# Kernel tuning notes

Hardware: AMD Instinct MI355X
Metric: run time of the kernel (lower is better)

Reference implementation:

```python
import jax, jax.numpy as jnp
import numpy as np

NUM_SECTIONS = 8192
EMBED_DIM = 768
NUM_HEADS = 12
D_K = 64
TOTAL_DIM = NUM_HEADS * D_K  # 768
M_MISSING = 2048
N_EXIST = 6144


def setup_inputs() -> dict:
    key = jax.random.key(0)
    ks = jax.random.split(key, 9)
    ehr = jax.random.normal(ks[0], (NUM_SECTIONS, EMBED_DIM), dtype=jnp.float32)
    # disjoint split of section indices (as in real missing/existing sections)
    perm = jax.random.permutation(ks[1], NUM_SECTIONS)
    missing_indices = perm[:M_MISSING].astype(jnp.int64) if jax.config.jax_enable_x64 else perm[:M_MISSING].astype(jnp.int32)
    exist_indices = perm[M_MISSING:M_MISSING + N_EXIST].astype(missing_indices.dtype)
    s = 1.0 / np.sqrt(EMBED_DIM)
    Wq = jax.random.normal(ks[2], (EMBED_DIM, TOTAL_DIM), dtype=jnp.float32) * s
    Wk = jax.random.normal(ks[3], (EMBED_DIM, TOTAL_DIM), dtype=jnp.float32) * s
    Wv = jax.random.normal(ks[4], (EMBED_DIM, TOTAL_DIM), dtype=jnp.float32) * s
    bq = jax.random.normal(ks[5], (TOTAL_DIM,), dtype=jnp.float32) * 0.01
    bk = jax.random.normal(ks[6], (TOTAL_DIM,), dtype=jnp.float32) * 0.01
    bv = jax.random.normal(ks[7], (TOTAL_DIM,), dtype=jnp.float32) * 0.01
    cooc_bias = jax.random.normal(ks[8], (NUM_HEADS, NUM_SECTIONS, D_K), dtype=jnp.float32)
    return {"ehr_embeddings": ehr, "exist_indices": exist_indices,
            "missing_indices": missing_indices, "Wq": Wq, "bq": bq,
            "Wk": Wk, "bk": bk, "Wv": Wv, "bv": bv, "cooc_bias": cooc_bias}


def reference(ehr_embeddings, exist_indices, missing_indices, Wq, bq, Wk, bk, Wv, bv, cooc_bias):
    M = missing_indices.shape[0]
    N = exist_indices.shape[0]
    missing_emb = ehr_embeddings[missing_indices]   # [M, E]
    exist_emb = ehr_embeddings[exist_indices]       # [N, E]
    # Q/K/V projections, split into heads: [H, M|N, d_k]
    q = (missing_emb @ Wq + bq).reshape(M, NUM_HEADS, D_K).transpose(1, 0, 2)
    k = (exist_emb @ Wk + bk).reshape(N, NUM_HEADS, D_K).transpose(1, 0, 2)
    v = (exist_emb @ Wv + bv).reshape(N, NUM_HEADS, D_K).transpose(1, 0, 2)
    scores = jnp.einsum('hmd,hnd->hmn', q, k) / jnp.sqrt(jnp.float32(D_K))
    # learned section co-occurrence bias
    missing_bias = cooc_bias[:, missing_indices, :]  # [H, M, d_k]
    exist_bias = cooc_bias[:, exist_indices, :]      # [H, N, d_k]
    scores = scores + jnp.einsum('hmd,hnd->hmn', missing_bias, exist_bias)
    attn = jax.nn.softmax(scores, axis=-1)
    out = jnp.einsum('hmn,hnd->hmd', attn, v)        # [H, M, d_k]
    out = out.transpose(1, 0, 2).reshape(M, TOTAL_DIM)
    return ehr_embeddings.at[missing_indices].set(out)
```

## Files before the change

### kernel.cpp

```cpp
#include <hip/hip_runtime.h>

typedef __attribute__((ext_vector_type(8))) short short8;
typedef __attribute__((ext_vector_type(8))) _Float16 half8;
typedef __attribute__((ext_vector_type(4))) float f32x4;
typedef __attribute__((ext_vector_type(16))) float f32x16;
typedef __attribute__((ext_vector_type(4))) unsigned short us4;
typedef __attribute__((ext_vector_type(4))) unsigned int u32x4;

#define MFMA16(a,b,c)  __builtin_amdgcn_mfma_f32_16x16x32_bf16(a,b,c,0,0,0)
#define MFMA32(a,b,c)  __builtin_amdgcn_mfma_f32_32x32x16_bf16(a,b,c,0,0,0)
#define MFMA32H(a,b,c) __builtin_amdgcn_mfma_f32_32x32x16_f16(a,b,c,0,0,0)

#define EMBED 768
#define HEADS 12
#define DK 64
#define M_MISS 2048
#define N_EX 6144
#define NSEC 8192
#define DPHY 128
#define QSC 0.125f
#define THR 7.0f

#define GLOAD16(g, l) __builtin_amdgcn_global_load_lds( \
    (const __attribute__((address_space(1))) unsigned int*)(g), \
    (__attribute__((address_space(3))) unsigned int*)(l), 16, 0, 0)

__device__ __forceinline__ unsigned short f2bf(float f){
  unsigned u = __builtin_bit_cast(unsigned, f);
  u += 0x7FFFu + ((u >> 16) & 1u);
  return (unsigned short)(u >> 16);
}
__device__ __forceinline__ unsigned short f2h(float f){
  _Float16 h = (_Float16)f;
  return __builtin_bit_cast(unsigned short, h);
}
__device__ __forceinline__ float max3(float a, float b, float c){
  return fmaxf(fmaxf(a, b), c);
}

__global__ __launch_bounds__(256) void k_setup(
    const float* __restrict__ ehr, unsigned short* __restrict__ ehrb,
    const float* __restrict__ Wq, const float* __restrict__ Wk,
    const float* __restrict__ Wv, unsigned short* __restrict__ Wt)
{
  __shared__ float tile[64][65];
  int b = blockIdx.x, tid = threadIdx.x;
  if (b < 3072) {
    long g = (long)b * 256 + tid;
    float4 v0 = *reinterpret_cast<const float4*>(&ehr[g * 8]);
    float4 v1 = *reinterpret_cast<const float4*>(&ehr[g * 8 + 4]);
    short8 p;
    p[0]=(short)f2bf(v0.x); p[1]=(short)f2bf(v0.y); p[2]=(short)f2bf(v0.z); p[3]=(short)f2bf(v0.w);
    p[4]=(short)f2bf(v1.x); p[5]=(short)f2bf(v1.y); p[6]=(short)f2bf(v1.z); p[7]=(short)f2bf(v1.w);
    *reinterpret_cast<short8*>(&ehrb[g * 8]) = p;
    return;
  }
  int bid = b - 3072;
  int which = bid / 144, t = bid % 144;
  int er0 = (t / 12) * 64, cc0 = (t % 12) * 64;
  const float* W = (which == 0) ? Wq : ((which == 1) ? Wk : Wv);
  unsigned short* dst = Wt + (long)which * EMBED * EMBED;
  {
    int e = tid >> 4, c4 = (tid & 15) * 4;
    for (int i = 0; i < 4; i++) {
      float4 v = *reinterpret_cast<const float4*>(&W[(long)(er0 + e + i*16) * EMBED + cc0 + c4]);
      tile[e + i*16][c4 + 0] = v.x; tile[e + i*16][c4 + 1] = v.y;
      tile[e + i*16][c4 + 2] = v.z; tile[e + i*16][c4 + 3] = v.w;
    }
  }
  __syncthreads();
  {
    int c = tid >> 4, e4 = (tid & 15) * 4;
    for (int i = 0; i < 4; i++) {
      us4 u;
      for (int j = 0; j < 4; j++) u[j] = f2bf(tile[e4 + j][c + i*16]);
      *reinterpret_cast<us4*>(&dst[(long)(cc0 + c + i*16) * EMBED + er0 + e4]) = u;
    }
  }
}

__global__ __launch_bounds__(256) void k_gemm_fused(
    const unsigned short* __restrict__ ehrb,
    const int* __restrict__ missing, const int* __restrict__ exist,
    const unsigned short* __restrict__ Wt,
    const float* __restrict__ bq, const float* __restrict__ bk, const float* __restrict__ bv,
    unsigned short* __restrict__ Qp, unsigned short* __restrict__ Kp, unsigned short* __restrict__ Vt,
    const float* __restrict__ cooc, const float* __restrict__ ehr, float* __restrict__ out)
{
  __shared__ unsigned char sA[2][8192];
  __shared__ unsigned char sB[2][8192];
  int bid = blockIdx.x;
  int tid = threadIdx.x;

  if (bid >= 6816) {
    int t4 = (bid - 6816) * 4 + (tid >> 6);
    long row = exist[t4];
    const f32x4* s = reinterpret_cast<const f32x4*>(ehr + row * EMBED);
    f32x4* d = reinterpret_cast<f32x4*>(out + row * EMBED);
    int l = tid & 63;
    d[l] = s[l]; d[l + 64] = s[l + 64]; d[l + 128] = s[l + 128];
    return;
  }
  if (bid >= 672) {
    const int* idx; unsigned short* dst; int count; int g;
    if (bid < 2208) { idx = missing; dst = Qp; count = M_MISS; g = (bid -  672) * 256 + tid; }
    else            { idx = exist;   dst = Kp; count = N_EX;   g = (bid - 2208) * 256 + tid; }
    int d4 = (g & 15) * 4;
    int r  = (g >> 4) % count;
    int h  = (g >> 4) / count;
    int src_row = idx[r];
    float4 v = *reinterpret_cast<const float4*>(&cooc[((long)h * NSEC + src_row) * DK + d4]);
    us4 hf;
    hf[0] = f2h(v.x); hf[1] = f2h(v.y); hf[2] = f2h(v.z); hf[3] = f2h(v.w);
    long base = ((long)h * count + r) * DPHY;
    *reinterpret_cast<us4*>(&dst[base + 64 + d4]) = hf;
    return;
  }

  int mode, row0, col0;
  const int* idx; const unsigned short* W; const float* bias;
  if (bid < 96)       { mode = 0; idx = missing; W = Wt;              bias = bq;
                        row0 = (bid & 15) * 128; col0 = (bid >> 4) * 128; }
  else if (bid < 384) { int t = bid - 96;  mode = 1; idx = exist; W = Wt + 589824;     bias = bk;
                        row0 = (t % 48) * 128; col0 = (t / 48) * 128; }
  else                { int t = bid - 384; mode = 2; idx = exist; W = Wt + 2 * 589824; bias = bv;
                        row0 = (t % 48) * 128; col0 = (t / 48) * 128; }

  int wv4 = tid >> 6, lane = tid & 63, l15 = lane & 15, lg = lane >> 4;
  int wm = wv4 >> 1, wn = wv4 & 1;

  int ar = tid >> 2, sl = tid & 3;
  int aoff = (sl ^ (ar & 3)) << 3;
  long gA0 = (long)idx[row0 + ar] * EMBED + aoff;
  long gA1 = (long)idx[row0 + ar + 64] * EMBED + aoff;
  long gB0 = (long)(col0 + ar) * EMBED + aoff;
  long gB1 = gB0 + (long)64 * EMBED;

  f32x4 acc[4][4];
  #pragma unroll
  for (int i = 0; i < 4; i++)
    #pragma unroll
    for (int j = 0; j < 4; j++) acc[i][j] = (f32x4){0.f,0.f,0.f,0.f};

  #define STAGE_G(buf, k0) do { \
    GLOAD16(ehrb + gA0 + (k0), &sA[buf][wv4 * 1024]); \
    GLOAD16(ehrb + gA1 + (k0), &sA[buf][4096 + wv4 * 1024]); \
    GLOAD16(W + gB0 + (k0), &sB[buf][wv4 * 1024]); \
    GLOAD16(W + gB1 + (k0), &sB[buf][4096 + wv4 * 1024]); \
  } while (0)

  STAGE_G(0, 0);
  __syncthreads();
  int cur = 0;
  for (int ks = 0; ks < 24; ks++) {
    if (ks < 23) STAGE_G(cur ^ 1, (ks + 1) * 32);
    short8 a[4], b[4];
    #pragma unroll
    for (int i = 0; i < 4; i++) {
      unsigned r = (unsigned)(wm * 64 + 16 * i + l15);
      a[i] = *reinterpret_cast<const short8*>(&sA[cur][r * 64 + (((unsigned)lg ^ (r & 3)) << 4)]);
      unsigned c = (unsigned)(wn * 64 + 16 * i + l15);
      b[i] = *reinterpret_cast<const short8*>(&sB[cur][c * 64 + (((unsigned)lg ^ (c & 3)) << 4)]);
    }
    #pragma unroll
    for (int i = 0; i < 4; i++)
      #pragma unroll
      for (int j = 0; j < 4; j++)
        acc[i][j] = MFMA16(a[i], b[j], acc[i][j]);
    __syncthreads();
    cur ^= 1;
  }
  #undef STAGE_G

  #pragma unroll
  for (int i = 0; i < 4; i++) {
    int mrow = row0 + wm * 64 + 16 * i + lg * 4;
    #pragma unroll
    for (int j = 0; j < 4; j++) {
      int cg = col0 + wn * 64 + 16 * j + l15;
      float bv_ = bias[cg];
      int h = cg >> 6, d = cg & 63;
      if (mode == 2) {
        us4 u;
        #pragma unroll
        for (int r = 0; r < 4; r++) u[r] = f2bf(acc[i][j][r] + bv_);
        *reinterpret_cast<us4*>(&Vt[((long)h * 64 + d) * N_EX + mrow]) = u;
      } else if (mode == 0) {
        #pragma unroll
        for (int r = 0; r < 4; r++)
          Qp[((long)h * M_MISS + mrow + r) * DPHY + d] = f2bf((acc[i][j][r] + bv_) * QSC);
      } else {
        #pragma unroll
        for (int r = 0; r < 4; r++)
          Kp[((long)h * N_EX + mrow + r) * DPHY + d] = f2bf(acc[i][j][r] + bv_);
      }
    }
  }
}

template<int NS>
__global__ __launch_bounds__(256, 3) void k_attn(
    const unsigned short* __restrict__ Qp, const unsigned short* __restrict__ Kp,
    const unsigned short* __restrict__ Vt,
    float* __restrict__ Opart, float* __restrict__ ML)
{
  constexpr int NSLc = N_EX / NS;
  constexpr int ITERS = NSLc / 64;
  int cpx = 24 * NS;
  int wg = (blockIdx.x & 7) * cpx + (blockIdx.x >> 3);
  int per_h = NS << 4;
  int h  = wg / per_h;
  int rem = wg - h * per_h;
  int sp = rem >> 4;
  int qb = rem & 15;
  int tid = threadIdx.x;
  int wv = tid >> 6, lane = tid & 63, l31 = lane & 31, hh = lane >> 5;

  __shared__ unsigned char sK[64 * 256];
  __shared__ unsigned char sV[64 * 128];

  int koff[4];
  #pragma unroll
  for (int i = 0; i < 4; i++) {
    int s = i * 256 + tid;
    int row = s >> 4, slt = s & 15;
    koff[i] = row * DPHY + ((slt ^ (row & 15)) << 3);
  }
  int voff[2];
  #pragma unroll
  for (int i = 0; i < 2; i++) {
    int s = i * 256 + tid;
    int row = s >> 3, slt = s & 7;
    voff[i] = row * N_EX + ((slt ^ (row & 7)) << 3);
  }
  const unsigned short* kti0 = Kp + ((long)h * N_EX + sp * NSLc) * DPHY;
  const unsigned short* vti0 = Vt + (long)h * 64 * N_EX + sp * NSLc;

  int mbase = qb * 128 + wv * 32;
  int m = mbase + l31;

  short8 qg[8];
  {
    const unsigned short* qrow = Qp + ((long)h * M_MISS + m) * DPHY + hh * 8;
    #pragma unroll
    for (int g = 0; g < 8; g++)
      qg[g] = *reinterpret_cast<const short8*>(qrow + g * 16);
  }

  f32x16 oacc[2];
  #pragma unroll
  for (int dt = 0; dt < 2; dt++)
    #pragma unroll
    for (int r = 0; r < 16; r++) oacc[dt][r] = 0.f;
  float m_run = -3.0e38f, l_run = 0.f;

  for (int it = 0; it < ITERS; ++it) {
    __syncthreads();
    {
      const unsigned short* kt_ = kti0 + (long)it * 64 * DPHY;
      GLOAD16(kt_ + koff[0], &sK[(0 * 4 + wv) * 1024]);
      GLOAD16(kt_ + koff[1], &sK[(1 * 4 + wv) * 1024]);
      GLOAD16(kt_ + koff[2], &sK[(2 * 4 + wv) * 1024]);
      GLOAD16(kt_ + koff[3], &sK[(3 * 4 + wv) * 1024]);
      const unsigned short* vt_ = vti0 + it * 64;
      GLOAD16(vt_ + voff[0], &sV[(0 * 4 + wv) * 1024]);
      GLOAD16(vt_ + voff[1], &sV[(1 * 4 + wv) * 1024]);
    }
    __syncthreads();

    f32x16 st[2];
    #pragma unroll
    for (int nt = 0; nt < 2; nt++) {
      #pragma unroll
      for (int r = 0; r < 16; r++) st[nt][r] = 0.f;
      unsigned nrow = (unsigned)(nt * 32 + l31);
      const unsigned char* kb = &sK[nrow * 256];
      unsigned px = nrow & 15;
      #define KRD(g) (*reinterpret_cast<const short8*>(kb + ((((unsigned)(2*(g)+hh)) ^ px) << 4)))
      short8 kf;
      kf = KRD(0); st[nt] = MFMA32(kf, qg[0], st[nt]);
      kf = KRD(1); st[nt] = MFMA32(kf, qg[1], st[nt]);
      kf = KRD(2); st[nt] = MFMA32(kf, qg[2], st[nt]);
      kf = KRD(3); st[nt] = MFMA32(kf, qg[3], st[nt]);
      kf = KRD(4); st[nt] = MFMA32H(__builtin_bit_cast(half8, kf), __builtin_bit_cast(half8, qg[4]), st[nt]);
      kf = KRD(5); st[nt] = MFMA32H(__builtin_bit_cast(half8, kf), __builtin_bit_cast(half8, qg[5]), st[nt]);
      kf = KRD(6); st[nt] = MFMA32H(__builtin_bit_cast(half8, kf), __builtin_bit_cast(half8, qg[6]), st[nt]);
      kf = KRD(7); st[nt] = MFMA32H(__builtin_bit_cast(half8, kf), __builtin_bit_cast(half8, qg[7]), st[nt]);
      #undef KRD
    }

    float t0 = max3(max3(st[0][0],  st[0][1],  st[0][2]),
                    max3(st[0][3],  st[0][4],  st[0][5]),
                    max3(st[0][6],  st[0][7],  st[0][8]));
    float t1 = max3(max3(st[0][9],  st[0][10], st[0][11]),
                    max3(st[0][12], st[0][13], st[0][14]),
                    max3(st[0][15], st[1][0],  st[1][1]));
    float t2 = max3(max3(st[1][2],  st[1][3],  st[1][4]),
                    max3(st[1][5],  st[1][6],  st[1][7]),
                    max3(st[1][8],  st[1][9],  st[1][10]));
    float t3 = max3(max3(st[1][11], st[1][12], st[1][13]),
                    fmaxf(st[1][14], st[1][15]), t0);
    float mx = max3(t1, t2, t3);
    mx = fmaxf(mx, __shfl_xor(mx, 32));
    if (!__all(mx <= m_run + THR)) {
      float mn = fmaxf(m_run, mx);
      float sc = __expf(m_run - mn);
      m_run = mn;
      l_run *= sc;
      #pragma unroll
      for (int dt = 0; dt < 2; dt++)
        #pragma unroll
        for (int r = 0; r < 16; r++) oacc[dt][r] *= sc;
    }
    float lsum = 0.f;
    unsigned c[2][4][2];
    #pragma unroll
    for (int nt = 0; nt < 2; nt++) {
      float p[16];
      #pragma unroll
      for (int r = 0; r < 16; r++) { p[r] = __expf(st[nt][r] - m_run); lsum += p[r]; }
      #pragma unroll
      for (int jj = 0; jj < 4; jj++) {
        asm("v_cvt_pk_bf16_f32 %0, %1, %2" : "=v"(c[nt][jj][0]) : "v"(p[4*jj+0]), "v"(p[4*jj+1]));
        asm("v_cvt_pk_bf16_f32 %0, %1, %2" : "=v"(c[nt][jj][1]) : "v"(p[4*jj+2]), "v"(p[4*jj+3]));
      }
    }
    lsum += __shfl_xor(lsum, 32);
    l_run += lsum;

    short8 pf[2][2];
    #pragma unroll
    for (int nt = 0; nt < 2; nt++)
      #pragma unroll
      for (int ks = 0; ks < 2; ks++) {
        unsigned a0 = c[nt][2*ks][0], b0 = c[nt][2*ks+1][0];
        unsigned a1 = c[nt][2*ks][1], b1 = c[nt][2*ks+1][1];
        asm("v_permlane32_swap_b32 %0, %1" : "+v"(a0), "+v"(b0));
        asm("v_permlane32_swap_b32 %0, %1" : "+v"(a1), "+v"(b1));
        u32x4 w;
        w[0] = a0; w[1] = a1; w[2] = b0; w[3] = b1;
        pf[nt][ks] = __builtin_bit_cast(short8, w);
      }

    #pragma unroll
    for (int dt = 0; dt < 2; dt++) {
      unsigned drow = (unsigned)(dt * 32 + l31);
      const unsigned char* vb = &sV[drow * 128];
      unsigned pd = drow & 7;
      #pragma unroll
      for (int nt = 0; nt < 2; nt++)
        #pragma unroll
        for (int ks = 0; ks < 2; ks++) {
          short8 vf = *reinterpret_cast<const short8*>(vb + ((((unsigned)(nt*4+ks*2+hh)) ^ pd) << 4));
          oacc[dt] = MFMA32(vf, pf[nt][ks], oacc[dt]);
        }
    }
  }

  long pbase = ((long)(h * NS + sp)) * M_MISS;
  if (hh == 0) {
    float2 v; v.x = m_run; v.y = l_run;
    *reinterpret_cast<float2*>(&ML[(pbase + m) * 2]) = v;
  }
  #pragma unroll
  for (int dt = 0; dt < 2; dt++)
    #pragma unroll
    for (int rq = 0; rq < 4; rq++) {
      f32x4 o4;
      o4[0] = oacc[dt][4*rq + 0]; o4[1] = oacc[dt][4*rq + 1];
      o4[2] = oacc[dt][4*rq + 2]; o4[3] = oacc[dt][4*rq + 3];
      *reinterpret_cast<f32x4*>(&Opart[(pbase + m) * 64 + dt * 32 + 8 * rq + 4 * hh]) = o4;
    }
}

__global__ __launch_bounds__(256) void k_merge(
    const float* __restrict__ Opart, const float* __restrict__ ML,
    const int* __restrict__ missing, float* __restrict__ out, int ns)
{
  int g = blockIdx.x * 256 + threadIdx.x;
  int d4 = (g & 15) * 4;
  int row = g >> 4;
  int m = row & (M_MISS - 1), h = row >> 11;
  long b0 = (long)h * ns * M_MISS + m;
  float M = -3.0e38f;
  for (int sp = 0; sp < ns; sp++)
    M = fmaxf(M, ML[(b0 + (long)sp * M_MISS) * 2]);
  float L = 0.f;
  f32x4 o = (f32x4){0.f,0.f,0.f,0.f};
  for (int sp = 0; sp < ns; sp++) {
    float2 v = *reinterpret_cast<const float2*>(&ML[(b0 + (long)sp * M_MISS) * 2]);
    float w = __expf(v.x - M);
    L += v.y * w;
    f32x4 t = *reinterpret_cast<const f32x4*>(&Opart[(b0 + (long)sp * M_MISS) * 64 + d4]);
    o += t * w;
  }
  float inv = 1.0f / L;
  int orow = missing[m];
  *reinterpret_cast<f32x4*>(&out[(long)orow * EMBED + h * 64 + d4]) = o * inv;
}

extern "C" void kernel_launch(void* const* d_in, const int* in_sizes, int n_in,
                              void* d_out, int out_size, void* d_ws, size_t ws_size,
                              hipStream_t stream) {
  const float* ehr     = (const float*)d_in[0];
  const int*   exist   = (const int*)  d_in[1];
  const int*   missing = (const int*)  d_in[2];
  const float* Wq = (const float*)d_in[3];
  const float* bq = (const float*)d_in[4];
  const float* Wk = (const float*)d_in[5];
  const float* bk = (const float*)d_in[6];
  const float* Wv = (const float*)d_in[7];
  const float* bv = (const float*)d_in[8];
  const float* cooc = (const float*)d_in[9];
  float* out = (float*)d_out;

  const int ns = 4;

  char* ws = (char*)d_ws;
  size_t opB = (size_t)HEADS * ns * M_MISS * 64 * 4;
  unsigned short* Wt   = (unsigned short*)(ws);
  unsigned short* ehrb = (unsigned short*)(ws + 3538944);
  float*          Op   = (float*)(ws);
  unsigned short* Qp = (unsigned short*)(ws + opB);
  unsigned short* Kp = (unsigned short*)(ws + opB + 6291456);
  unsigned short* Vt = (unsigned short*)(ws + opB + 25165824);
  float*          Ml = (float*)(ws + opB + 34603008);

  k_setup<<<3504, 256, 0, stream>>>(ehr, ehrb, Wq, Wk, Wv, Wt);
  k_gemm_fused<<<8352, 256, 0, stream>>>(ehrb, missing, exist, Wt, bq, bk, bv,
                                         Qp, Kp, Vt, cooc, ehr, out);
  k_attn<4><<<HEADS * 4 * 16, 256, 0, stream>>>(Qp, Kp, Vt, Op, Ml);
  k_merge<<<HEADS * M_MISS * 16 / 256, 256, 0, stream>>>(Op, Ml, missing, out, ns);
}
```

Measured before the change: 125.1 us.

## Double-buffer K/V shared-memory tiles to overlap loads with MFMA compute

Splits the K and V LDS tiles into two buffers and prefetches the next iteration's tiles with direct global-to-LDS loads while the current tile is being processed. This replaces two barriers per iteration with one and hides global load latency behind the QK and PV matrix work. It doubles LDS use per block, which could lower occupancy under the three-blocks-per-CU target.

Result: no change. 126.5 us (+1.1%).

```diff
diff --git a/kernel.cpp b/kernel.cpp
--- a/kernel.cpp
+++ b/kernel.cpp
@@ -216,8 +216,8 @@
   int tid = threadIdx.x;
   int wv = tid >> 6, lane = tid & 63, l31 = lane & 31, hh = lane >> 5;
 
-  __shared__ unsigned char sK[64 * 256];
-  __shared__ unsigned char sV[64 * 128];
+  __shared__ unsigned char sK[2][64 * 256];
+  __shared__ unsigned char sV[2][64 * 128];
 
   int koff[4];
   #pragma unroll
@@ -236,6 +236,17 @@
   const unsigned short* kti0 = Kp + ((long)h * N_EX + sp * NSLc) * DPHY;
   const unsigned short* vti0 = Vt + (long)h * 64 * N_EX + sp * NSLc;
 
+  #define STAGE_KV(buf, it) do { \
+    const unsigned short* kt_ = kti0 + (long)(it) * 64 * DPHY; \
+    GLOAD16(kt_ + koff[0], &sK[buf][(0 * 4 + wv) * 1024]); \
+    GLOAD16(kt_ + koff[1], &sK[buf][(1 * 4 + wv) * 1024]); \
+    GLOAD16(kt_ + koff[2], &sK[buf][(2 * 4 + wv) * 1024]); \
+    GLOAD16(kt_ + koff[3], &sK[buf][(3 * 4 + wv) * 1024]); \
+    const unsigned short* vt_ = vti0 + (it) * 64; \
+    GLOAD16(vt_ + voff[0], &sV[buf][(0 * 4 + wv) * 1024]); \
+    GLOAD16(vt_ + voff[1], &sV[buf][(1 * 4 + wv) * 1024]); \
+  } while (0)
+
   int mbase = qb * 128 + wv * 32;
   int m = mbase + l31;
 
@@ -254,19 +265,12 @@
     for (int r = 0; r < 16; r++) oacc[dt][r] = 0.f;
   float m_run = -3.0e38f, l_run = 0.f;
 
+  STAGE_KV(0, 0);
+  __syncthreads();
+  int cur = 0;
+
   for (int it = 0; it < ITERS; ++it) {
-    __syncthreads();
-    {
-      const unsigned short* kt_ = kti0 + (long)it * 64 * DPHY;
-      GLOAD16(kt_ + koff[0], &sK[(0 * 4 + wv) * 1024]);
-      GLOAD16(kt_ + koff[1], &sK[(1 * 4 + wv) * 1024]);
-      GLOAD16(kt_ + koff[2], &sK[(2 * 4 + wv) * 1024]);
-      GLOAD16(kt_ + koff[3], &sK[(3 * 4 + wv) * 1024]);
-      const unsigned short* vt_ = vti0 + it * 64;
-      GLOAD16(vt_ + voff[0], &sV[(0 * 4 + wv) * 1024]);
-      GLOAD16(vt_ + voff[1], &sV[(1 * 4 + wv) * 1024]);
-    }
-    __syncthreads();
+    if (it + 1 < ITERS) STAGE_KV(cur ^ 1, it + 1);
 
     f32x16 st[2];
     #pragma unroll
@@ -274,7 +278,7 @@
       #pragma unroll
       for (int r = 0; r < 16; r++) st[nt][r] = 0.f;
       unsigned nrow = (unsigned)(nt * 32 + l31);
-      const unsigned char* kb = &sK[nrow * 256];
+      const unsigned char* kb = &sK[cur][nrow * 256];
       unsigned px = nrow & 15;
       #define KRD(g) (*reinterpret_cast<const short8*>(kb + ((((unsigned)(2*(g)+hh)) ^ px) << 4)))
       short8 kf;
@@ -345,7 +349,7 @@
     #pragma unroll
     for (int dt = 0; dt < 2; dt++) {
       unsigned drow = (unsigned)(dt * 32 + l31);
-      const unsigned char* vb = &sV[drow * 128];
+      const unsigned char* vb = &sV[cur][drow * 128];
       unsigned pd = drow & 7;
       #pragma unroll
       for (int nt = 0; nt < 2; nt++)
@@ -355,7 +359,11 @@
           oacc[dt] = MFMA32(vf, pf[nt][ks], oacc[dt]);
         }
     }
-  }
+
+    __syncthreads();
+    cur ^= 1;
+  }
+  #undef STAGE_KV
 
   long pbase = ((long)(h * NS + sp)) * M_MISS;
   if (hh == 0) {
```
